# Kernel optimization log

Hardware: AMD Instinct MI355X
Metric: run time of the kernel (lower is better)

## Reference

```python
import jax, jax.numpy as jnp
import numpy as np

H = 16
D_MODEL = 1024
D_K = D_MODEL // H
B, S = 8, 1024


def setup_inputs() -> dict:
    key = jax.random.key(0)
    ks = jax.random.split(key, 11)
    scale = 1.0 / np.sqrt(D_MODEL)
    inp = {
        "query": jax.random.normal(ks[0], (B, S, D_MODEL), jnp.float32),
        "key_": jax.random.normal(ks[1], (B, S, D_MODEL), jnp.float32),
        "value": jax.random.normal(ks[2], (B, S, D_MODEL), jnp.float32),
        "w_q": jax.random.normal(ks[3], (D_MODEL, D_MODEL), jnp.float32) * scale,
        "b_q": jnp.zeros((D_MODEL,), jnp.float32),
        "w_k": jax.random.normal(ks[4], (D_MODEL, D_MODEL), jnp.float32) * scale,
        "b_k": jnp.zeros((D_MODEL,), jnp.float32),
        "w_v": jax.random.normal(ks[5], (D_MODEL, D_MODEL), jnp.float32) * scale,
        "b_v": jnp.zeros((D_MODEL,), jnp.float32),
        "w_o": jax.random.normal(ks[6], (D_MODEL, D_MODEL), jnp.float32) * scale,
        "b_o": jnp.zeros((D_MODEL,), jnp.float32),
    }
    return inp


def reference(query, key_, value, w_q, b_q, w_k, b_k, w_v, b_v, w_o, b_o):
    # Linear projections (torch Linear: x @ W.T + b), then split heads: [B,S,D] -> [B,H,S,d_k]
    def proj(x, w, b):
        y = jnp.einsum("bsd,ed->bse", x, w) + b
        return y.reshape(B, S, H, D_K).transpose(0, 2, 1, 3)

    q = proj(query, w_q, b_q)
    k = proj(key_, w_k, b_k)
    v = proj(value, w_v, b_v)

    # Scaled dot-product attention (mask=None, dropout p=0 -> identity)
    scores = jnp.einsum("bhqd,bhkd->bhqk", q, k) / jnp.sqrt(jnp.float32(D_K))
    attn = jax.nn.softmax(scores, axis=-1)
    ctx = jnp.einsum("bhqk,bhkd->bhqd", attn, v)  # [B,H,S,d_k]

    # Merge heads and final output projection
    ctx = ctx.transpose(0, 2, 1, 3).reshape(B, S, D_MODEL)
    return jnp.einsum("bsd,ed->bse", ctx, w_o) + b_o
```

## Files before the change

kernel.cpp:

```cpp
#include <hip/hip_runtime.h>
#include <hip/hip_bf16.h>

#define NH 16
#define DK 64
#define BB 8
#define SS 1024
#define DM 1024
#define MTOT (BB * SS)

typedef float f4v __attribute__((ext_vector_type(4)));
typedef float f16v __attribute__((ext_vector_type(16)));
typedef short s16v8 __attribute__((ext_vector_type(8)));
typedef unsigned short u16v4 __attribute__((ext_vector_type(4)));
typedef unsigned short u16v8 __attribute__((ext_vector_type(8)));

#define EXP2F(x) __builtin_amdgcn_exp2f(x)

__device__ __forceinline__ unsigned short f2bf(float x) {
    unsigned int u = __float_as_uint(x);
    u += 0x7FFFu + ((u >> 16) & 1u);
    return (unsigned short)(u >> 16);
}

__device__ __forceinline__ unsigned int packbf2(float lo, float hi) {
    return ((unsigned int)f2bf(hi) << 16) | f2bf(lo);
}

__device__ __forceinline__ void gload16(const void* g, void* l) {
    __builtin_amdgcn_global_load_lds(
        (const __attribute__((address_space(1))) void*)g,
        (__attribute__((address_space(3))) void*)l, 16, 0, 0);
}

struct Src7 { const float* p[7]; };

__global__ __launch_bounds__(256) void cvt_all(Src7 sp, unsigned short* __restrict__ dst) {
    const size_t e = ((size_t)blockIdx.x * 256 + threadIdx.x) * 8;
    const int unit = (int)(e >> 20);
    int t; size_t base;
    if (unit < 8)       { t = 0; base = 0; }
    else if (unit < 16) { t = 1; base = (size_t)8 << 20; }
    else if (unit < 24) { t = 2; base = (size_t)16 << 20; }
    else                { t = 3 + (unit - 24); base = (size_t)unit << 20; }
    const float* s = sp.p[t] + (e - base);
    f4v a = *(const f4v*)s;
    f4v b = *(const f4v*)(s + 4);
    u16v8 o;
    o[0] = f2bf(a[0]); o[1] = f2bf(a[1]); o[2] = f2bf(a[2]); o[3] = f2bf(a[3]);
    o[4] = f2bf(b[0]); o[5] = f2bf(b[1]); o[6] = f2bf(b[2]); o[7] = f2bf(b[3]);
    *(u16v8*)(dst + e) = o;
}

struct QkvArgs {
    const unsigned short* X[3];
    const unsigned short* W[3];
    const float* bias[3];
    unsigned short* Y[3];
};

__global__ __launch_bounds__(256) void gemm_qkv(QkvArgs a) {
    __shared__ unsigned short As[128 * 32];
    __shared__ unsigned short Bs[128 * 32];
    const int z = blockIdx.z;
    const unsigned short* X = a.X[z];
    const unsigned short* W = a.W[z];
    const float* bias = a.bias[z];
    unsigned short* Y = a.Y[z];

    const int tid = threadIdx.x;
    const int wv = tid >> 6, l = tid & 63;
    const int lq = l & 15, g = l >> 4;
    const int wr = wv >> 1, wc = wv & 1;
    const int m0 = blockIdx.x * 128, n0 = blockIdx.y * 128;

    f4v acc[4][4];
#pragma unroll
    for (int i = 0; i < 4; ++i)
#pragma unroll
        for (int j = 0; j < 4; ++j) acc[i][j] = (f4v){0.f, 0.f, 0.f, 0.f};

    for (int kt = 0; kt < DM / 32; ++kt) {
        const int k0 = kt * 32;
        __syncthreads();
#pragma unroll
        for (int p = 0; p < 2; ++p) {
            const int u = p * 256 + tid;
            const int row = u >> 2, kc = u & 3;
            gload16(X + (size_t)(m0 + row) * DM + k0 + kc * 8, As + (size_t)u * 8);
            gload16(W + (size_t)(n0 + row) * DM + k0 + kc * 8, Bs + (size_t)u * 8);
        }
        __syncthreads();

        s16v8 av[4], bv[4];
#pragma unroll
        for (int i = 0; i < 4; ++i)
            av[i] = *(const s16v8*)(As + (wr * 64 + i * 16 + lq) * 32 + g * 8);
#pragma unroll
        for (int j = 0; j < 4; ++j)
            bv[j] = *(const s16v8*)(Bs + (wc * 64 + j * 16 + lq) * 32 + g * 8);
#pragma unroll
        for (int i = 0; i < 4; ++i)
#pragma unroll
            for (int j = 0; j < 4; ++j)
                acc[i][j] = __builtin_amdgcn_mfma_f32_16x16x32_bf16(av[i], bv[j], acc[i][j], 0, 0, 0);
    }

#pragma unroll
    for (int j = 0; j < 4; ++j) {
        const int col = n0 + wc * 64 + j * 16 + lq;
        const float bvl = bias[col];
#pragma unroll
        for (int i = 0; i < 4; ++i) {
            const int row0 = m0 + wr * 64 + i * 16 + g * 4;
            if (z < 2) {
#pragma unroll
                for (int r = 0; r < 4; ++r) {
                    const int row = row0 + r;
                    const int b_ = row >> 10, s_ = row & (SS - 1);
                    const int h_ = col >> 6, d_ = col & (DK - 1);
                    Y[((size_t)(b_ * NH + h_) * SS + s_) * DK + d_] = f2bf(acc[i][j][r] + bvl);
                }
            } else {
                const int b_ = row0 >> 10, s0_ = row0 & (SS - 1);
                const int h_ = col >> 6, d_ = col & (DK - 1);
                u16v4 o;
#pragma unroll
                for (int r = 0; r < 4; ++r) o[r] = f2bf(acc[i][j][r] + bvl);
                *(u16v4*)&Y[((size_t)(b_ * NH + h_) * DK + d_) * SS + s0_] = o;
            }
        }
    }
}

__global__ __launch_bounds__(256) void gemm_out(const unsigned short* __restrict__ X,
                                                const unsigned short* __restrict__ W,
                                                const float* __restrict__ bias,
                                                float* __restrict__ Y) {
    __shared__ unsigned short As[128 * 32];
    __shared__ unsigned short Bs[128 * 32];
    const int tid = threadIdx.x;
    const int wv = tid >> 6, l = tid & 63;
    const int lq = l & 15, g = l >> 4;
    const int wr = wv >> 1, wc = wv & 1;
    const int m0 = blockIdx.x * 128, n0 = blockIdx.y * 128;

    f4v acc[4][4];
#pragma unroll
    for (int i = 0; i < 4; ++i)
#pragma unroll
        for (int j = 0; j < 4; ++j) acc[i][j] = (f4v){0.f, 0.f, 0.f, 0.f};

    for (int kt = 0; kt < DM / 32; ++kt) {
        const int k0 = kt * 32;
        __syncthreads();
#pragma unroll
        for (int p = 0; p < 2; ++p) {
            const int u = p * 256 + tid;
            const int row = u >> 2, kc = u & 3;
            gload16(X + (size_t)(m0 + row) * DM + k0 + kc * 8, As + (size_t)u * 8);
            gload16(W + (size_t)(n0 + row) * DM + k0 + kc * 8, Bs + (size_t)u * 8);
        }
        __syncthreads();

        s16v8 av[4], bv[4];
#pragma unroll
        for (int i = 0; i < 4; ++i)
            av[i] = *(const s16v8*)(As + (wr * 64 + i * 16 + lq) * 32 + g * 8);
#pragma unroll
        for (int j = 0; j < 4; ++j)
            bv[j] = *(const s16v8*)(Bs + (wc * 64 + j * 16 + lq) * 32 + g * 8);
#pragma unroll
        for (int i = 0; i < 4; ++i)
#pragma unroll
            for (int j = 0; j < 4; ++j)
                acc[i][j] = __builtin_amdgcn_mfma_f32_16x16x32_bf16(av[i], bv[j], acc[i][j], 0, 0, 0);
    }

#pragma unroll
    for (int j = 0; j < 4; ++j) {
        const int col = n0 + wc * 64 + j * 16 + lq;
        const float bvl = bias[col];
#pragma unroll
        for (int i = 0; i < 4; ++i) {
#pragma unroll
            for (int r = 0; r < 4; ++r) {
                const int row = m0 + wr * 64 + i * 16 + g * 4 + r;
                Y[(size_t)row * DM + col] = acc[i][j][r] + bvl;
            }
        }
    }
}

__device__ __forceinline__ void attn_iter(int t, int tn,
                                          const unsigned short* __restrict__ Kb,
                                          const unsigned short* __restrict__ Vb,
                                          int l31, int hi,
                                          const s16v8 (&qf)[4],
                                          s16v8 (&ku)[2][4],
                                          s16v8 (&kl)[2][4],
                                          f16v& O0, f16v& O1, float& me, float& lr) {
    const float C = 0.18033688011112042f;

    s16v8 vf[2][4];
#pragma unroll
    for (int db = 0; db < 2; ++db)
#pragma unroll
        for (int ksg = 0; ksg < 4; ++ksg)
            vf[db][ksg] = *(const s16v8*)(Vb + (size_t)(db * 32 + l31) * SS + t * 64 + ksg * 16 + hi * 8);
#pragma unroll
    for (int ks = 0; ks < 2; ++ks)
#pragma unroll
        for (int kd = 0; kd < 4; ++kd)
            kl[ks][kd] = *(const s16v8*)(Kb + (size_t)(tn * 64 + ks * 32 + l31) * DK + kd * 16 + hi * 8);

    f16v s0, s1;
#pragma unroll
    for (int r = 0; r < 16; ++r) { s0[r] = 0.f; s1[r] = 0.f; }
#pragma unroll
    for (int kd = 0; kd < 4; ++kd) {
        s0 = __builtin_amdgcn_mfma_f32_32x32x16_bf16(ku[0][kd], qf[kd], s0, 0, 0, 0);
        s1 = __builtin_amdgcn_mfma_f32_32x32x16_bf16(ku[1][kd], qf[kd], s1, 0, 0, 0);
    }

    float mx = s0[0];
#pragma unroll
    for (int r = 1; r < 16; ++r) mx = fmaxf(mx, s0[r]);
#pragma unroll
    for (int r = 0; r < 16; ++r) mx = fmaxf(mx, s1[r]);
    mx = fmaxf(mx, __shfl_xor(mx, 32));
    const float mxl = mx * C;

    const bool need = !__all(mxl - me <= 8.0f);
    float corr = 1.0f;
    if (need) {
        const float mnew = fmaxf(me, mxl);
        corr = EXP2F(me - mnew);
        me = mnew;
    }

    float rs = 0.f;
#pragma unroll
    for (int r = 0; r < 16; ++r) { s0[r] = EXP2F(__fmaf_rn(s0[r], C, -me)); rs += s0[r]; }
#pragma unroll
    for (int r = 0; r < 16; ++r) { s1[r] = EXP2F(__fmaf_rn(s1[r], C, -me)); rs += s1[r]; }
    rs += __shfl_xor(rs, 32);
    if (need) {
        lr = lr * corr + rs;
#pragma unroll
        for (int r = 0; r < 16; ++r) { O0[r] *= corr; O1[r] *= corr; }
    } else {
        lr += rs;
    }

    s16v8 pb[2][2];
#pragma unroll
    for (int ks = 0; ks < 2; ++ks) {
        unsigned int u[8], su[8];
#pragma unroll
        for (int i = 0; i < 8; ++i) {
            const float plo = (ks == 0) ? s0[2 * i] : s1[2 * i];
            const float phi = (ks == 0) ? s0[2 * i + 1] : s1[2 * i + 1];
            u[i] = packbf2(plo, phi);
        }
#pragma unroll
        for (int i = 0; i < 8; ++i) su[i] = (unsigned int)__shfl_xor((int)u[i], 32);
#pragma unroll
        for (int kk = 0; kk < 2; ++kk) {
            const int base = 4 * kk + 2 * hi;
            union { unsigned int w[4]; s16v8 s; } f;
            f.w[0] = hi ? su[base] : u[base];
            f.w[1] = hi ? su[base + 1] : u[base + 1];
            f.w[2] = hi ? u[base] : su[base];
            f.w[3] = hi ? u[base + 1] : su[base + 1];
            pb[ks][kk] = f.s;
        }
    }

#pragma unroll
    for (int ksg = 0; ksg < 4; ++ksg) {
        O0 = __builtin_amdgcn_mfma_f32_32x32x16_bf16(vf[0][ksg], pb[ksg >> 1][ksg & 1], O0, 0, 0, 0);
        O1 = __builtin_amdgcn_mfma_f32_32x32x16_bf16(vf[1][ksg], pb[ksg >> 1][ksg & 1], O1, 0, 0, 0);
    }
}

__global__ __launch_bounds__(256, 2) void attn_mfma32(const unsigned short* __restrict__ Qp,
                                                      const unsigned short* __restrict__ Kp,
                                                      const unsigned short* __restrict__ Vt,
                                                      unsigned short* __restrict__ ctx) {
    __shared__ unsigned short Ob[4][2048];
    const int tid = threadIdx.x;
    const int wv = tid >> 6;
    const int l = tid & 63;
    const int l31 = l & 31, hi = l >> 5;
    const int bh = blockIdx.x;
    const int qblk = blockIdx.y;
    const int q = qblk * 128 + wv * 32 + l31;

    const unsigned short* Qrow = Qp + ((size_t)bh * SS + q) * DK + hi * 8;
    s16v8 qf[4];
#pragma unroll
    for (int kd = 0; kd < 4; ++kd) qf[kd] = *(const s16v8*)(Qrow + kd * 16);

    const unsigned short* Kb = Kp + (size_t)bh * SS * DK;
    const unsigned short* Vb = Vt + (size_t)bh * DK * SS;

    f16v O0, O1;
#pragma unroll
    for (int r = 0; r < 16; ++r) { O0[r] = 0.f; O1[r] = 0.f; }
    float me = -1e30f;
    float lr = 0.f;

    s16v8 kA[2][4], kB[2][4];
#pragma unroll
    for (int ks = 0; ks < 2; ++ks)
#pragma unroll
        for (int kd = 0; kd < 4; ++kd)
            kA[ks][kd] = *(const s16v8*)(Kb + (size_t)(ks * 32 + l31) * DK + kd * 16 + hi * 8);

    for (int tt = 0; tt < 8; ++tt) {
        const int t0 = 2 * tt, t1 = 2 * tt + 1;
        attn_iter(t0, t1, Kb, Vb, l31, hi, qf, kA, kB, O0, O1, me, lr);
        attn_iter(t1, (t1 + 1 < 16) ? t1 + 1 : 15, Kb, Vb, l31, hi, qf, kB, kA, O0, O1, me, lr);
    }

    const float inv = 1.0f / lr;
    unsigned short* mybuf = Ob[wv];
#pragma unroll
    for (int db = 0; db < 2; ++db) {
        const f16v Ocur = db ? O1 : O0;
#pragma unroll
        for (int g2 = 0; g2 < 4; ++g2) {
            uint2 w;
            w.x = packbf2(Ocur[4 * g2 + 0] * inv, Ocur[4 * g2 + 1] * inv);
            w.y = packbf2(Ocur[4 * g2 + 2] * inv, Ocur[4 * g2 + 3] * inv);
            const int off = db * 64 + g2 * 16 + hi * 8;
            *(uint2*)((char*)mybuf + l31 * 128 + (off ^ ((l31 & 7) << 4))) = w;
        }
    }
    __syncthreads();

    const int r = l >> 1, h2 = l & 1;
    const int qrow = qblk * 128 + wv * 32 + r;
    const int b_ = bh >> 4, h_ = bh & 15;
    unsigned short* crow = ctx + ((size_t)b_ * SS + qrow) * DM + h_ * DK + h2 * 32;
#pragma unroll
    for (int j = 0; j < 4; ++j) {
        const int off = (h2 * 64 + j * 16) ^ ((r & 7) << 4);
        u16v8 v = *(const u16v8*)((const char*)mybuf + r * 128 + off);
        *(u16v8*)(crow + j * 8) = v;
    }
}

extern "C" void kernel_launch(void* const* d_in, const int* in_sizes, int n_in,
                              void* d_out, int out_size, void* d_ws, size_t ws_size,
                              hipStream_t stream) {
    const float* query = (const float*)d_in[0];
    const float* key_  = (const float*)d_in[1];
    const float* value = (const float*)d_in[2];
    const float* w_q = (const float*)d_in[3];
    const float* b_q = (const float*)d_in[4];
    const float* w_k = (const float*)d_in[5];
    const float* b_k = (const float*)d_in[6];
    const float* w_v = (const float*)d_in[7];
    const float* b_v = (const float*)d_in[8];
    const float* w_o = (const float*)d_in[9];
    const float* b_o = (const float*)d_in[10];

    unsigned short* ws = (unsigned short*)d_ws;
    const size_t NX = (size_t)MTOT * DM;
    const size_t NW = (size_t)DM * DM;
    unsigned short* xq  = ws;
    unsigned short* xk  = xq + NX;
    unsigned short* xv  = xk + NX;
    unsigned short* wqb = xv + NX;
    unsigned short* wkb = wqb + NW;
    unsigned short* wvb = wkb + NW;
    unsigned short* wob = wvb + NW;
    unsigned short* Qp  = wob + NW;
    unsigned short* Kp  = Qp + NX;
    unsigned short* VpT = Kp + NX;
    unsigned short* ctx = xq;

    Src7 sp;
    sp.p[0] = query; sp.p[1] = key_; sp.p[2] = value;
    sp.p[3] = w_q; sp.p[4] = w_k; sp.p[5] = w_v; sp.p[6] = w_o;
    cvt_all<<<14336, 256, 0, stream>>>(sp, ws);

    QkvArgs qa;
    qa.X[0] = xq;  qa.X[1] = xk;  qa.X[2] = xv;
    qa.W[0] = wqb; qa.W[1] = wkb; qa.W[2] = wvb;
    qa.bias[0] = b_q; qa.bias[1] = b_k; qa.bias[2] = b_v;
    qa.Y[0] = Qp; qa.Y[1] = Kp; qa.Y[2] = VpT;
    gemm_qkv<<<dim3(MTOT / 128, DM / 128, 3), 256, 0, stream>>>(qa);

    attn_mfma32<<<dim3(BB * NH, SS / 128), 256, 0, stream>>>(Qp, Kp, VpT, ctx);

    gemm_out<<<dim3(MTOT / 128, DM / 128), 256, 0, stream>>>(ctx, wob, b_o, (float*)d_out);
}
```

Measured before the change: 423.8 us.

## Stage K/V tiles through double-buffered LDS with async loads in attention

The attention kernel previously had every wave load its own K and V fragments straight from global memory into registers. Now a 512-thread block (8 waves, 256 queries) cooperatively copies each 64-key K/V tile into LDS with async global-to-LDS loads. The copies are double-buffered so the next tile's transfer overlaps the current tile's MFMA and softmax work. This cuts redundant global/L2 traffic by sharing tiles across more waves, but adds two barriers per tile and raw waitcnt encodings that must match the hardware counters.

```diff
diff --git a/kernel.cpp b/kernel.cpp
--- a/kernel.cpp
+++ b/kernel.cpp
@@ -15,6 +15,8 @@
 typedef unsigned short u16v8 __attribute__((ext_vector_type(8)));
 
 #define EXP2F(x) __builtin_amdgcn_exp2f(x)
+#define WAIT_VM2() __builtin_amdgcn_s_waitcnt(0x0F72)
+#define WAIT_VM0() __builtin_amdgcn_s_waitcnt(0x0F70)
 
 __device__ __forceinline__ unsigned short f2bf(float x) {
     unsigned int u = __float_as_uint(x);
@@ -191,110 +193,22 @@
     }
 }
 
-__device__ __forceinline__ void attn_iter(int t, int tn,
-                                          const unsigned short* __restrict__ Kb,
-                                          const unsigned short* __restrict__ Vb,
-                                          int l31, int hi,
-                                          const s16v8 (&qf)[4],
-                                          s16v8 (&ku)[2][4],
-                                          s16v8 (&kl)[2][4],
-                                          f16v& O0, f16v& O1, float& me, float& lr) {
-    const float C = 0.18033688011112042f;
-
-    s16v8 vf[2][4];
-#pragma unroll
-    for (int db = 0; db < 2; ++db)
-#pragma unroll
-        for (int ksg = 0; ksg < 4; ++ksg)
-            vf[db][ksg] = *(const s16v8*)(Vb + (size_t)(db * 32 + l31) * SS + t * 64 + ksg * 16 + hi * 8);
-#pragma unroll
-    for (int ks = 0; ks < 2; ++ks)
-#pragma unroll
-        for (int kd = 0; kd < 4; ++kd)
-            kl[ks][kd] = *(const s16v8*)(Kb + (size_t)(tn * 64 + ks * 32 + l31) * DK + kd * 16 + hi * 8);
-
-    f16v s0, s1;
-#pragma unroll
-    for (int r = 0; r < 16; ++r) { s0[r] = 0.f; s1[r] = 0.f; }
-#pragma unroll
-    for (int kd = 0; kd < 4; ++kd) {
-        s0 = __builtin_amdgcn_mfma_f32_32x32x16_bf16(ku[0][kd], qf[kd], s0, 0, 0, 0);
-        s1 = __builtin_amdgcn_mfma_f32_32x32x16_bf16(ku[1][kd], qf[kd], s1, 0, 0, 0);
-    }
-
-    float mx = s0[0];
-#pragma unroll
-    for (int r = 1; r < 16; ++r) mx = fmaxf(mx, s0[r]);
-#pragma unroll
-    for (int r = 0; r < 16; ++r) mx = fmaxf(mx, s1[r]);
-    mx = fmaxf(mx, __shfl_xor(mx, 32));
-    const float mxl = mx * C;
-
-    const bool need = !__all(mxl - me <= 8.0f);
-    float corr = 1.0f;
-    if (need) {
-        const float mnew = fmaxf(me, mxl);
-        corr = EXP2F(me - mnew);
-        me = mnew;
-    }
-
-    float rs = 0.f;
-#pragma unroll
-    for (int r = 0; r < 16; ++r) { s0[r] = EXP2F(__fmaf_rn(s0[r], C, -me)); rs += s0[r]; }
-#pragma unroll
-    for (int r = 0; r < 16; ++r) { s1[r] = EXP2F(__fmaf_rn(s1[r], C, -me)); rs += s1[r]; }
-    rs += __shfl_xor(rs, 32);
-    if (need) {
-        lr = lr * corr + rs;
-#pragma unroll
-        for (int r = 0; r < 16; ++r) { O0[r] *= corr; O1[r] *= corr; }
-    } else {
-        lr += rs;
-    }
-
-    s16v8 pb[2][2];
-#pragma unroll
-    for (int ks = 0; ks < 2; ++ks) {
-        unsigned int u[8], su[8];
-#pragma unroll
-        for (int i = 0; i < 8; ++i) {
-            const float plo = (ks == 0) ? s0[2 * i] : s1[2 * i];
-            const float phi = (ks == 0) ? s0[2 * i + 1] : s1[2 * i + 1];
-            u[i] = packbf2(plo, phi);
-        }
-#pragma unroll
-        for (int i = 0; i < 8; ++i) su[i] = (unsigned int)__shfl_xor((int)u[i], 32);
-#pragma unroll
-        for (int kk = 0; kk < 2; ++kk) {
-            const int base = 4 * kk + 2 * hi;
-            union { unsigned int w[4]; s16v8 s; } f;
-            f.w[0] = hi ? su[base] : u[base];
-            f.w[1] = hi ? su[base + 1] : u[base + 1];
-            f.w[2] = hi ? u[base] : su[base];
-            f.w[3] = hi ? u[base + 1] : su[base + 1];
-            pb[ks][kk] = f.s;
-        }
-    }
-
-#pragma unroll
-    for (int ksg = 0; ksg < 4; ++ksg) {
-        O0 = __builtin_amdgcn_mfma_f32_32x32x16_bf16(vf[0][ksg], pb[ksg >> 1][ksg & 1], O0, 0, 0, 0);
-        O1 = __builtin_amdgcn_mfma_f32_32x32x16_bf16(vf[1][ksg], pb[ksg >> 1][ksg & 1], O1, 0, 0, 0);
-    }
-}
-
-__global__ __launch_bounds__(256, 2) void attn_mfma32(const unsigned short* __restrict__ Qp,
+__global__ __launch_bounds__(512, 4) void attn_mfma32(const unsigned short* __restrict__ Qp,
                                                       const unsigned short* __restrict__ Kp,
                                                       const unsigned short* __restrict__ Vt,
                                                       unsigned short* __restrict__ ctx) {
-    __shared__ unsigned short Ob[4][2048];
+    __shared__ unsigned short Sh[16384];
     const int tid = threadIdx.x;
     const int wv = tid >> 6;
     const int l = tid & 63;
     const int l31 = l & 31, hi = l >> 5;
     const int bh = blockIdx.x;
     const int qblk = blockIdx.y;
-    const int q = qblk * 128 + wv * 32 + l31;
+    const int q = qblk * 256 + wv * 32 + l31;
+    const float C = 0.18033688011112042f;
+
+#define ShK(buf) (Sh + (buf) * 4096)
+#define ShV(buf) (Sh + 8192 + (buf) * 4096)
 
     const unsigned short* Qrow = Qp + ((size_t)bh * SS + q) * DK + hi * 8;
     s16v8 qf[4];
@@ -303,6 +217,15 @@
 
     const unsigned short* Kb = Kp + (size_t)bh * SS * DK;
     const unsigned short* Vb = Vt + (size_t)bh * DK * SS;
+
+#define STAGE(buf, t)                                                       \
+    {                                                                       \
+        const int u = tid;                                                  \
+        gload16(Kb + (size_t)((t) * 64 + (u & 63)) * DK + (u >> 6) * 8,     \
+                ShK(buf) + (size_t)u * 8);                                  \
+        gload16(Vb + (size_t)(u & 63) * SS + (t) * 64 + (u >> 6) * 8,       \
+                ShV(buf) + (size_t)u * 8);                                  \
+    }
 
     f16v O0, O1;
 #pragma unroll
@@ -310,21 +233,107 @@
     float me = -1e30f;
     float lr = 0.f;
 
-    s16v8 kA[2][4], kB[2][4];
-#pragma unroll
-    for (int ks = 0; ks < 2; ++ks)
-#pragma unroll
-        for (int kd = 0; kd < 4; ++kd)
-            kA[ks][kd] = *(const s16v8*)(Kb + (size_t)(ks * 32 + l31) * DK + kd * 16 + hi * 8);
-
-    for (int tt = 0; tt < 8; ++tt) {
-        const int t0 = 2 * tt, t1 = 2 * tt + 1;
-        attn_iter(t0, t1, Kb, Vb, l31, hi, qf, kA, kB, O0, O1, me, lr);
-        attn_iter(t1, (t1 + 1 < 16) ? t1 + 1 : 15, Kb, Vb, l31, hi, qf, kB, kA, O0, O1, me, lr);
-    }
+    STAGE(0, 0);
+    int cur = 0;
+
+    for (int t = 0; t < SS / 64; ++t) {
+        const int tn = (t < SS / 64 - 1) ? t + 1 : t;
+        STAGE(cur ^ 1, tn);
+        WAIT_VM2();
+        __builtin_amdgcn_s_barrier();
+
+        s16v8 kf[2][4];
+#pragma unroll
+        for (int ks = 0; ks < 2; ++ks)
+#pragma unroll
+            for (int kd = 0; kd < 4; ++kd)
+                kf[ks][kd] = *(const s16v8*)(ShK(cur) + (((2 * kd + hi) * 64) + ks * 32 + l31) * 8);
+        s16v8 vf[2][4];
+#pragma unroll
+        for (int db = 0; db < 2; ++db)
+#pragma unroll
+            for (int ksg = 0; ksg < 4; ++ksg)
+                vf[db][ksg] = *(const s16v8*)(ShV(cur) + (((2 * ksg + hi) * 64) + db * 32 + l31) * 8);
+
+        f16v s0, s1;
+#pragma unroll
+        for (int r = 0; r < 16; ++r) { s0[r] = 0.f; s1[r] = 0.f; }
+#pragma unroll
+        for (int kd = 0; kd < 4; ++kd) {
+            s0 = __builtin_amdgcn_mfma_f32_32x32x16_bf16(kf[0][kd], qf[kd], s0, 0, 0, 0);
+            s1 = __builtin_amdgcn_mfma_f32_32x32x16_bf16(kf[1][kd], qf[kd], s1, 0, 0, 0);
+        }
+
+        float mx = s0[0];
+#pragma unroll
+        for (int r = 1; r < 16; ++r) mx = fmaxf(mx, s0[r]);
+#pragma unroll
+        for (int r = 0; r < 16; ++r) mx = fmaxf(mx, s1[r]);
+        mx = fmaxf(mx, __shfl_xor(mx, 32));
+        const float mxl = mx * C;
+
+        const bool need = !__all(mxl - me <= 8.0f);
+        float corr = 1.0f;
+        if (need) {
+            const float mnew = fmaxf(me, mxl);
+            corr = EXP2F(me - mnew);
+            me = mnew;
+        }
+
+        float rs = 0.f;
+#pragma unroll
+        for (int r = 0; r < 16; ++r) { s0[r] = EXP2F(__fmaf_rn(s0[r], C, -me)); rs += s0[r]; }
+#pragma unroll
+        for (int r = 0; r < 16; ++r) { s1[r] = EXP2F(__fmaf_rn(s1[r], C, -me)); rs += s1[r]; }
+        rs += __shfl_xor(rs, 32);
+        if (need) {
+            lr = lr * corr + rs;
+#pragma unroll
+            for (int r = 0; r < 16; ++r) { O0[r] *= corr; O1[r] *= corr; }
+        } else {
+            lr += rs;
+        }
+
+        s16v8 pb[2][2];
+#pragma unroll
+        for (int ks = 0; ks < 2; ++ks) {
+            unsigned int u[8], su[8];
+#pragma unroll
+            for (int i = 0; i < 8; ++i) {
+                const float plo = (ks == 0) ? s0[2 * i] : s1[2 * i];
+                const float phi = (ks == 0) ? s0[2 * i + 1] : s1[2 * i + 1];
+                u[i] = packbf2(plo, phi);
+            }
+#pragma unroll
+            for (int i = 0; i < 8; ++i) su[i] = (unsigned int)__shfl_xor((int)u[i], 32);
+#pragma unroll
+            for (int kk = 0; kk < 2; ++kk) {
+                const int base = 4 * kk + 2 * hi;
+                union { unsigned int w[4]; s16v8 s; } f;
+                f.w[0] = hi ? su[base] : u[base];
+                f.w[1] = hi ? su[base + 1] : u[base + 1];
+                f.w[2] = hi ? u[base] : su[base];
+                f.w[3] = hi ? u[base + 1] : su[base + 1];
+                pb[ks][kk] = f.s;
+            }
+        }
+
+#pragma unroll
+        for (int ksg = 0; ksg < 4; ++ksg) {
+            O0 = __builtin_amdgcn_mfma_f32_32x32x16_bf16(vf[0][ksg], pb[ksg >> 1][ksg & 1], O0, 0, 0, 0);
+            O1 = __builtin_amdgcn_mfma_f32_32x32x16_bf16(vf[1][ksg], pb[ksg >> 1][ksg & 1], O1, 0, 0, 0);
+        }
+
+        __builtin_amdgcn_s_barrier();
+        cur ^= 1;
+    }
+#undef STAGE
+
+    WAIT_VM0();
+    __builtin_amdgcn_s_barrier();
 
     const float inv = 1.0f / lr;
-    unsigned short* mybuf = Ob[wv];
+    unsigned short* mybuf = Sh + wv * 2048;
 #pragma unroll
     for (int db = 0; db < 2; ++db) {
         const f16v Ocur = db ? O1 : O0;
@@ -340,7 +349,7 @@
     __syncthreads();
 
     const int r = l >> 1, h2 = l & 1;
-    const int qrow = qblk * 128 + wv * 32 + r;
+    const int qrow = qblk * 256 + wv * 32 + r;
     const int b_ = bh >> 4, h_ = bh & 15;
     unsigned short* crow = ctx + ((size_t)b_ * SS + qrow) * DM + h_ * DK + h2 * 32;
 #pragma unroll
@@ -349,6 +358,8 @@
         u16v8 v = *(const u16v8*)((const char*)mybuf + r * 128 + off);
         *(u16v8*)(crow + j * 8) = v;
     }
+#undef ShK
+#undef ShV
 }
 
 extern "C" void kernel_launch(void* const* d_in, const int* in_sizes, int n_in,
@@ -393,7 +404,7 @@
     qa.Y[0] = Qp; qa.Y[1] = Kp; qa.Y[2] = VpT;
     gemm_qkv<<<dim3(MTOT / 128, DM / 128, 3), 256, 0, stream>>>(qa);
 
-    attn_mfma32<<<dim3(BB * NH, SS / 128), 256, 0, stream>>>(Qp, Kp, VpT, ctx);
+    attn_mfma32<<<dim3(BB * NH, SS / 256), 512, 0, stream>>>(Qp, Kp, VpT, ctx);
 
     gemm_out<<<dim3(MTOT / 128, DM / 128), 256, 0, stream>>>(ctx, wob, b_o, (float*)d_out);
 }
```

Measured after the change: 362.9 us. 1.17x faster.
